# Kernel tuning notes

Measured on AMD Instinct MI355X. Metric: run time of the kernel, lower is better.

## Reference

```python
import jax, jax.numpy as jnp
import numpy as np

B = 4096      # batch (length of the per-sample python loop in the original)
H = 512       # lstm hidden size
A = 18        # nb_action
D = 1024 + A + 1   # lstm / env-embedding dim = 1043
M = 32768     # max_mem_len
K = 32        # ltm_query_breadth
EPS = 1e-5


def _ln(x, g, b):
    m = jnp.mean(x, axis=-1, keepdims=True)
    v = jnp.var(x, axis=-1, keepdims=True)
    return (x - m) / jnp.sqrt(v + EPS) * g + b


def _lstm_cell(x, h, c, W_ih, W_hh, bias):
    # gates: [B, 4H]; split order f, i, o, g (as in the torch module)
    gates = x @ W_ih + h @ W_hh + bias
    f, i, o, g = jnp.split(gates, 4, axis=1)
    c1 = jax.nn.sigmoid(f) * c + jax.nn.sigmoid(i) * jnp.tanh(g)
    h1 = jax.nn.sigmoid(o) * jnp.tanh(c1)
    return h1, c1


def setup_inputs() -> dict:
    key = jax.random.key(0)
    ks = jax.random.split(key, 14)
    f32 = jnp.float32
    return {
        "env_embeddings": jax.random.normal(ks[0], (B, D), f32),
        "hxs": 0.1 * jax.random.normal(ks[1], (B, H), f32),
        "cxs": 0.1 * jax.random.normal(ks[2], (B, H), f32),
        "mem_keys": jax.random.normal(ks[3], (M, H), f32),
        "mem_values": jax.random.normal(ks[4], (M, D), f32),
        "W_ih": 0.02 * jax.random.normal(ks[5], (D, 4 * H), f32),
        "W_hh": 0.02 * jax.random.normal(ks[6], (H, 4 * H), f32),
        "bias": jnp.zeros((4 * H,), f32),
        "ln_g": jnp.ones((H,), f32),
        "ln_b": jnp.zeros((H,), f32),
        "W_critic": 0.02 * jax.random.normal(ks[7], (H, 1), f32),
        "b_critic": jnp.zeros((1,), f32),
        "W_actor": 0.02 * jax.random.normal(ks[8], (H, A), f32),
        "b_actor": jnp.zeros((A,), f32),
        "k": K,
    }


def reference(env_embeddings, hxs, cxs, mem_keys, mem_values,
              W_ih, W_hh, bias, ln_g, ln_b,
              W_critic, b_critic, W_actor, b_actor, k):
    # --- first LSTM pass (batched; per-sample loop in torch is independent) ---
    h1, c1 = _lstm_cell(env_embeddings, hxs, cxs, W_ih, W_hh, bias)

    # --- LTM retrieval: query = layernorm(cell state), top-k attention over memory ---
    q = _ln(c1, ln_g, ln_b)                      # [B, H]
    scores = q @ mem_keys.T                      # [B, M]
    top_vals, inds = jax.lax.top_k(scores, k)    # [B, K]
    weights = jax.nn.softmax(top_vals, axis=-1)  # [B, K]
    gathered = mem_values[inds]                  # [B, K, D]
    memories = jnp.einsum('bk,bkd->bd', weights, gathered)  # [B, D]

    # --- second LSTM pass with retrieved memory as input ---
    h2, c2 = _lstm_cell(memories, h1, c1, W_ih, W_hh, bias)

    critic = h2 @ W_critic + b_critic            # [B, 1]
    actor = h2 @ W_actor + b_actor               # [B, A]
    return critic, actor, h2, c2, inds, weights
```

## Files before the change

kernel.cpp:

```cpp
#include <hip/hip_runtime.h>
#include <hip/hip_bf16.h>
#include <math.h>

#define BATCH 4096
#define HID   512
#define NACT  18
#define DIM   1043
#define MEMN  32768
#define TOPK  32
#define G4H   2048
#define NCHUNK 16
#define CHUNKM (MEMN / NCHUNK)
#define KCP   512

#define OFF_C1   0ull
#define OFF_Q    2097152ull
#define OFF_H1B  4194304ull
#define OFF_PV   5242880ull
#define OFF_PI   7340032ull
#define OFF_MEMB 5242880ull

#define OUT_CRITIC 0
#define OUT_ACTOR  4096
#define OUT_H2     77824
#define OUT_C2     2174976
#define OUT_INDS   4272128
#define OUT_W      4403200

__device__ __forceinline__ float toF_(float x) { return x; }
__device__ __forceinline__ float toF_(__hip_bfloat16 x) { return __bfloat162float(x); }
__device__ __forceinline__ float sigf_(float x) { return 1.0f / (1.0f + expf(-x)); }

__device__ __forceinline__ float np_expf(float x) {
  const float magic = 12582912.0f;
  float q = fmaf(x, 1.442695040888963f, magic) - magic;
  float r = fmaf(q, -6.93145752e-1f, x);
  r = fmaf(q, -1.42860677e-6f, r);
  float num = fmaf(5.082762527590693718096e-04f, r, 6.757896990527504603057e-03f);
  num = fmaf(num, r, 5.114512081637298353406e-02f);
  num = fmaf(num, r, 2.473615434895520810817e-01f);
  num = fmaf(num, r, 7.257664613233124478488e-01f);
  num = fmaf(num, r, 9.999999999980870924916e-01f);
  float den = fmaf(2.159509375685829852307e-02f, r, -2.742335390411667452936e-01f);
  den = fmaf(den, r, 1.0f);
  float poly = __fdiv_rn(num, den);
  int qi = (int)q;
  float scale = __uint_as_float((unsigned)(127 + qi) << 23);
  return __fmul_rn(poly, scale);
}
__device__ __forceinline__ float np_sigmoidf(float x) {
  const float e = np_expf(-x);
  return __fdiv_rn(1.0f, __fadd_rn(1.0f, e));
}
__device__ __forceinline__ float cr_tanhf(float x) { return (float)tanh((double)x); }

template<int PASS, typename TA, typename TC>
__global__ __launch_bounds__(512, 2) void gemm_lstm(
    const TA* __restrict__ A1, const TA* __restrict__ A2,
    const float* __restrict__ W1, const float* __restrict__ W2,
    const float* __restrict__ bias, const TC* __restrict__ cprev,
    float* __restrict__ c1out, __hip_bfloat16* __restrict__ h1b,
    float* __restrict__ outH2, float* __restrict__ outC2)
{
  __shared__ float as[32][66];
  __shared__ float bs[32][132];
  const int tid = threadIdx.x;
  const int b0 = blockIdx.y * 64;
  const int h0 = blockIdx.x * 32;
  const int tr = tid >> 5, tc = tid & 31;
  float accA[4][4] = {};
  float accB[4][4] = {};

  auto run = [&](const TA* __restrict__ A, const float* __restrict__ W,
                 int Ksz, float (&acc)[4][4]) {
    float accP[4][4] = {};
    for (int k0 = 0; k0 < Ksz; k0 += 32) {
      {
        const int r = tid >> 3, kq = tid & 7;
        #pragma unroll
        for (int j = 0; j < 4; ++j) {
          const int kidx = k0 + 4 * kq + j;
          as[4 * kq + j][r] =
              (kidx < Ksz) ? toF_(A[(size_t)(b0 + r) * Ksz + kidx]) : 0.0f;
        }
      }
      {
        const int kk = tid >> 4, sub = tid & 15;
        const bool ok = (k0 + kk) < Ksz;
        #pragma unroll
        for (int g = 0; g < 4; ++g)
          #pragma unroll
          for (int r2 = 0; r2 < 2; ++r2) {
            const float w =
                ok ? W[(size_t)(k0 + kk) * G4H + 512 * g + h0 + 2 * sub + r2] : 0.0f;
            bs[kk][(2 * sub + r2) * 4 + g] = w;
          }
      }
      __syncthreads();
      #pragma unroll
      for (int kk = 0; kk < 32; ++kk) {
        float a[4], b[4];
        #pragma unroll
        for (int u = 0; u < 4; ++u) a[u] = as[kk][4 * tr + u];
        #pragma unroll
        for (int u = 0; u < 4; ++u) b[u] = bs[kk][4 * tc + u];
        #pragma unroll
        for (int jj = 0; jj < 4; ++jj)
          #pragma unroll
          for (int g = 0; g < 4; ++g)
            accP[jj][g] = fmaf(a[jj], b[g], accP[jj][g]);
      }
      __syncthreads();
      if (((k0 + 32) % KCP == 0) || (k0 + 32 >= Ksz)) {
        #pragma unroll
        for (int jj = 0; jj < 4; ++jj)
          #pragma unroll
          for (int g = 0; g < 4; ++g) {
            acc[jj][g] = __fadd_rn(acc[jj][g], accP[jj][g]);
            accP[jj][g] = 0.0f;
          }
      }
    }
  };
  run(A1, W1, DIM, accA);
  run(A2, W2, HID, accB);

  const int h = h0 + tc;
  const float bf = bias[h];
  const float bi = bias[512 + h];
  const float bo = bias[1024 + h];
  const float bg = bias[1536 + h];
  #pragma unroll
  for (int jj = 0; jj < 4; ++jj) {
    const int b = b0 + 4 * tr + jj;
    const float fv = __fadd_rn(__fadd_rn(accA[jj][0], accB[jj][0]), bf);
    const float iv = __fadd_rn(__fadd_rn(accA[jj][1], accB[jj][1]), bi);
    const float ov = __fadd_rn(__fadd_rn(accA[jj][2], accB[jj][2]), bo);
    const float gv = __fadd_rn(__fadd_rn(accA[jj][3], accB[jj][3]), bg);
    const float cp = toF_(cprev[(size_t)b * HID + h]);
    if constexpr (PASS == 1) {
      const float sf = np_sigmoidf(fv);
      const float si = np_sigmoidf(iv);
      const float so = np_sigmoidf(ov);
      const float tg = cr_tanhf(gv);
      const float cn = __fadd_rn(__fmul_rn(sf, cp), __fmul_rn(si, tg));
      const float hn = __fmul_rn(so, cr_tanhf(cn));
      c1out[(size_t)b * HID + h] = cn;
      h1b[(size_t)b * HID + h] = __float2bfloat16(hn);
    } else {
      const float cn = sigf_(fv) * cp + sigf_(iv) * tanhf(gv);
      const float hn = sigf_(ov) * tanhf(cn);
      outC2[(size_t)b * HID + h] = cn;
      outH2[(size_t)b * HID + h] = hn;
    }
  }
}

__global__ __launch_bounds__(256) void ln_q_np(
    const float* __restrict__ c1, const float* __restrict__ ln_g,
    const float* __restrict__ ln_b, float* __restrict__ q)
{
  const int tid = threadIdx.x, lane = tid & 63;
  const int r = blockIdx.x * 4 + (tid >> 6);
  const float* c = c1 + (size_t)r * HID;

  float part;
  {
    const int bi = (lane & 31) >> 3, j = lane & 7;
    const float* p = c + bi * 128 + j;
    float s = p[0];
    #pragma unroll
    for (int k = 1; k < 16; ++k) s = __fadd_rn(s, p[8 * k]);
    part = s;
  }
  part = __fadd_rn(part, __shfl_xor(part, 1, 32));
  part = __fadd_rn(part, __shfl_xor(part, 2, 32));
  part = __fadd_rn(part, __shfl_xor(part, 4, 32));
  part = __fadd_rn(part, __shfl_xor(part, 8, 32));
  part = __fadd_rn(part, __shfl_xor(part, 16, 32));
  const float mean = __fmul_rn(part, 1.0f / 512.0f);

  float part2;
  {
    const int bi = (lane & 31) >> 3, j = lane & 7;
    const float* p = c + bi * 128 + j;
    float d = __fsub_rn(p[0], mean);
    float s = __fmul_rn(d, d);
    #pragma unroll
    for (int k = 1; k < 16; ++k) {
      d = __fsub_rn(p[8 * k], mean);
      s = __fadd_rn(s, __fmul_rn(d, d));
    }
    part2 = s;
  }
  part2 = __fadd_rn(part2, __shfl_xor(part2, 1, 32));
  part2 = __fadd_rn(part2, __shfl_xor(part2, 2, 32));
  part2 = __fadd_rn(part2, __shfl_xor(part2, 4, 32));
  part2 = __fadd_rn(part2, __shfl_xor(part2, 8, 32));
  part2 = __fadd_rn(part2, __shfl_xor(part2, 16, 32));
  const float var = __fmul_rn(part2, 1.0f / 512.0f);

  const float S = __fsqrt_rn(__fadd_rn(var, 1e-5f));
  #pragma unroll
  for (int u = 0; u < 8; ++u) {
    const int i = lane + 64 * u;
    const float dv = __fsub_rn(c[i], mean);
    q[(size_t)r * HID + i] =
        __fadd_rn(__fmul_rn(__fdiv_rn(dv, S), ln_g[i]), ln_b[i]);
  }
}

__global__ __launch_bounds__(512) void score_topk(
    const float* __restrict__ Q, const float* __restrict__ Km,
    float* __restrict__ pv, int* __restrict__ pi)
{
  __shared__ float qs[32][68];
  __shared__ float ks[32][132];
  const int tid = threadIdx.x;
  const int lane = tid & 63;
  const int b0 = blockIdx.y * 64;
  const int chunkBase = blockIdx.x * CHUNKM;
  const int tr = tid >> 5, tc = tid & 31;
  float listV[4];
  int   listI[4];
  #pragma unroll
  for (int j = 0; j < 4; ++j) { listV[j] = -INFINITY; listI[j] = 0; }

  for (int t = 0; t < CHUNKM / 128; ++t) {
    const int m0 = chunkBase + t * 128;
    float acc[4][4] = {};
    for (int k0 = 0; k0 < HID; k0 += 32) {
      {
        const int r = tid >> 3, kq = tid & 7;
        const float4 v = *(const float4*)(Q + (size_t)(b0 + r) * HID + k0 + 4 * kq);
        qs[4 * kq + 0][r] = v.x; qs[4 * kq + 1][r] = v.y;
        qs[4 * kq + 2][r] = v.z; qs[4 * kq + 3][r] = v.w;
      }
      {
        const int col = tid >> 2, sub = tid & 3;
        const float* kp = Km + (size_t)(m0 + col) * HID + k0 + 4 * sub;
        const float4 v0 = *(const float4*)kp;
        const float4 v1 = *(const float4*)(kp + 16);
        ks[4 * sub + 0][col] = v0.x; ks[4 * sub + 1][col] = v0.y;
        ks[4 * sub + 2][col] = v0.z; ks[4 * sub + 3][col] = v0.w;
        ks[16 + 4 * sub + 0][col] = v1.x; ks[16 + 4 * sub + 1][col] = v1.y;
        ks[16 + 4 * sub + 2][col] = v1.z; ks[16 + 4 * sub + 3][col] = v1.w;
      }
      __syncthreads();
      #pragma unroll
      for (int kk = 0; kk < 32; ++kk) {
        const float4 av = *(const float4*)&qs[kk][4 * tr];
        const float4 bv = *(const float4*)&ks[kk][4 * tc];
        const float a[4] = {av.x, av.y, av.z, av.w};
        const float b[4] = {bv.x, bv.y, bv.z, bv.w};
        #pragma unroll
        for (int jj = 0; jj < 4; ++jj)
          #pragma unroll
          for (int cc = 0; cc < 4; ++cc)
            acc[jj][cc] = fmaf(a[jj], b[cc], acc[jj][cc]);
      }
      __syncthreads();
    }
    #pragma unroll
    for (int j = 0; j < 4; ++j) {
      float thr = __shfl(listV[j], (lane < 32) ? 31 : 63);
      float ca[4];
      #pragma unroll
      for (int cc = 0; cc < 4; ++cc) ca[cc] = acc[j][cc];
      while (true) {
        const bool any = (ca[0] > thr) || (ca[1] > thr) ||
                         (ca[2] > thr) || (ca[3] > thr);
        unsigned long long m = __ballot(any);
        if (!m) break;
        const int src = __builtin_ctzll(m);
        const bool participate = ((lane >= 32) == (src >= 32));
        #pragma unroll
        for (int cc = 0; cc < 4; ++cc) {
          const float cv = __shfl(ca[cc], src);
          const float thr_src = __shfl(thr, src);
          if (cv > thr_src) {
            const int ci = m0 + 4 * (src & 31) + cc;
            const unsigned long long em =
                __ballot(participate && (listV[j] < cv));
            if (em) {
              const int pslot = __builtin_ctzll(em) & 31;
              const float shV = __shfl_up(listV[j], 1);
              const int  shI = __shfl_up(listI[j], 1);
              const int slot = lane & 31;
              if (participate && slot >= pslot) {
                listV[j] = (slot == pslot) ? cv : shV;
                listI[j] = (slot == pslot) ? ci : shI;
              }
              thr = __shfl(listV[j], (lane < 32) ? 31 : 63);
            }
          }
        }
        if (lane == src) { ca[0] = ca[1] = ca[2] = ca[3] = -INFINITY; }
      }
    }
  }
  #pragma unroll
  for (int j = 0; j < 4; ++j) {
    const int row = b0 + 8 * (tid >> 6) + j + ((lane >= 32) ? 4 : 0);
    const size_t o = ((size_t)row * NCHUNK + blockIdx.x) * TOPK + (lane & 31);
    pv[o] = listV[j];
    pi[o] = listI[j];
  }
}

__global__ __launch_bounds__(256) void merge_topk(
    const float* __restrict__ pv, const int* __restrict__ pi,
    float* __restrict__ outI, float* __restrict__ outW)
{
  const int tid = threadIdx.x;
  const int lane = tid & 63;
  const int b = blockIdx.x * 4 + (tid >> 6);
  float lv = -INFINITY;
  int li = 0;
  const size_t base = (size_t)b * (NCHUNK * TOPK);
  #pragma unroll
  for (int t = 0; t < (NCHUNK * TOPK) / 64; ++t) {
    const float v = pv[base + t * 64 + lane];
    const int ii = pi[base + t * 64 + lane];
    float thr = __shfl(lv, 31);
    unsigned long long m = __ballot(v > thr);
    while (m) {
      const int src = __builtin_ctzll(m);
      m &= (m - 1);
      const float cv = __shfl(v, src);
      const int ci = __shfl(ii, src);
      if (cv > thr) {
        const unsigned long long em = __ballot((lane < 32) && (lv < cv));
        if (em) {
          const int p = __builtin_ctzll(em);
          const float shV = __shfl_up(lv, 1);
          const int shI = __shfl_up(li, 1);
          if ((lane < 32) && lane >= p) {
            lv = (lane == p) ? cv : shV;
            li = (lane == p) ? ci : shI;
          }
          thr = __shfl(lv, 31);
        }
      }
    }
  }
  const float maxv = __shfl(lv, 0);
  float e = (lane < 32) ? expf(lv - maxv) : 0.0f;
  float s = e;
  #pragma unroll
  for (int d = 1; d < 64; d <<= 1) s += __shfl_xor(s, d);
  const float w = e / s;
  if (lane < 32) {
    outI[(size_t)b * TOPK + lane] = (float)li;
    outW[(size_t)b * TOPK + lane] = w;
  }
}

__global__ __launch_bounds__(256) void gather_mem(
    const float* __restrict__ wf, const float* __restrict__ inf_,
    const float* __restrict__ mv, __hip_bfloat16* __restrict__ memB)
{
  __shared__ float wl[TOPK];
  __shared__ int il[TOPK];
  const int b = blockIdx.x, tid = threadIdx.x;
  if (tid < TOPK) {
    wl[tid] = wf[(size_t)b * TOPK + tid];
    il[tid] = (int)inf_[(size_t)b * TOPK + tid];
  }
  __syncthreads();
  for (int c = tid; c < DIM; c += 256) {
    float acc = 0.0f;
    #pragma unroll
    for (int s = 0; s < TOPK; ++s)
      acc = fmaf(wl[s], mv[(size_t)il[s] * DIM + c], acc);
    memB[(size_t)b * DIM + c] = __float2bfloat16(acc);
  }
}

__global__ __launch_bounds__(256) void heads(
    const float* __restrict__ h2f,
    const float* __restrict__ Wc, const float* __restrict__ bc,
    const float* __restrict__ Wa, const float* __restrict__ ba,
    float* __restrict__ outC, float* __restrict__ outA)
{
  __shared__ float W[HID * 19];
  const int tid = threadIdx.x, lane = tid & 63, wid = tid >> 6;
  for (int idx = tid; idx < HID * 19; idx += 256) {
    const int l = idx / 19, o = idx % 19;
    W[idx] = (o < NACT) ? Wa[l * NACT + o] : Wc[l];
  }
  __syncthreads();
  const int r0 = blockIdx.x * 16 + wid * 4;
  for (int rr = 0; rr < 4; ++rr) {
    const int r = r0 + rr;
    float hv[8];
    #pragma unroll
    for (int u = 0; u < 8; ++u) hv[u] = h2f[(size_t)r * HID + lane + 64 * u];
    for (int o = 0; o < 19; ++o) {
      float s = 0.f;
      #pragma unroll
      for (int u = 0; u < 8; ++u) s = fmaf(hv[u], W[(lane + 64 * u) * 19 + o], s);
      #pragma unroll
      for (int d = 1; d < 64; d <<= 1) s += __shfl_xor(s, d);
      if (lane == 0) {
        if (o < NACT) outA[(size_t)r * NACT + o] = s + ba[o];
        else          outC[r] = s + bc[0];
      }
    }
  }
}

extern "C" void kernel_launch(void* const* d_in, const int* in_sizes, int n_in,
                              void* d_out, int out_size, void* d_ws, size_t ws_size,
                              hipStream_t stream) {
  (void)in_sizes; (void)n_in; (void)out_size; (void)ws_size;
  const float* env    = (const float*)d_in[0];
  const float* hxs    = (const float*)d_in[1];
  const float* cxs    = (const float*)d_in[2];
  const float* mkeys  = (const float*)d_in[3];
  const float* mvals  = (const float*)d_in[4];
  const float* W_ih   = (const float*)d_in[5];
  const float* W_hh   = (const float*)d_in[6];
  const float* bias   = (const float*)d_in[7];
  const float* ln_g   = (const float*)d_in[8];
  const float* ln_b   = (const float*)d_in[9];
  const float* Wc     = (const float*)d_in[10];
  const float* bc     = (const float*)d_in[11];
  const float* Wa     = (const float*)d_in[12];
  const float* ba     = (const float*)d_in[13];

  float* ws = (float*)d_ws;
  float* c1   = ws + OFF_C1;
  float* q    = ws + OFF_Q;
  __hip_bfloat16* h1b = (__hip_bfloat16*)(ws + OFF_H1B);
  float* pv   = ws + OFF_PV;
  int*   pi   = (int*)(ws + OFF_PI);
  __hip_bfloat16* memB = (__hip_bfloat16*)(ws + OFF_MEMB);
  float* out = (float*)d_out;

  gemm_lstm<1, float, float><<<dim3(HID / 32, BATCH / 64), 512, 0, stream>>>(
      env, hxs, W_ih, W_hh, bias, cxs, c1, h1b, nullptr, nullptr);
  ln_q_np<<<BATCH / 4, 256, 0, stream>>>(c1, ln_g, ln_b, q);
  score_topk<<<dim3(NCHUNK, BATCH / 64), 512, 0, stream>>>(q, mkeys, pv, pi);
  merge_topk<<<BATCH / 4, 256, 0, stream>>>(pv, pi, out + OUT_INDS, out + OUT_W);
  gather_mem<<<BATCH, 256, 0, stream>>>(out + OUT_W, out + OUT_INDS, mvals, memB);
  gemm_lstm<2, __hip_bfloat16, float>
      <<<dim3(HID / 32, BATCH / 64), 512, 0, stream>>>(
      memB, h1b, W_ih, W_hh, bias, c1, nullptr, nullptr,
      out + OUT_H2, out + OUT_C2);
  heads<<<BATCH / 16, 256, 0, stream>>>(out + OUT_H2, Wc, bc, Wa, ba,
                                        out + OUT_CRITIC, out + OUT_ACTOR);
}
```

Baseline: 3.995 ms.

## Enlarge score_topk tile to 128x256 with 8x8 register blocking per thread

The fused score+top-k kernel now processes 128 query rows by 256 memory keys per block, with each thread computing an 8x8 accumulator tile instead of 4x4. Shared-memory tiles are padded to avoid bank conflicts, and the per-row streaming top-k insertion logic is adapted to eight rows per half-wave. The aim is to raise FMA-to-LDS-load intensity and halve the global traffic for keys per query row. In exchange, register pressure rises to 64 accumulators plus 16 list registers, the grid halves to 512 blocks, and launch_bounds(512,4) may force spills.

```diff
diff --git a/kernel.cpp b/kernel.cpp
--- a/kernel.cpp
+++ b/kernel.cpp
@@ -210,78 +210,92 @@
   }
 }
 
-__global__ __launch_bounds__(512) void score_topk(
+__global__ __launch_bounds__(512, 4) void score_topk(
     const float* __restrict__ Q, const float* __restrict__ Km,
     float* __restrict__ pv, int* __restrict__ pi)
 {
-  __shared__ float qs[32][68];
-  __shared__ float ks[32][132];
+  __shared__ float as[32][132];
+  __shared__ float bs[32][288];
   const int tid = threadIdx.x;
   const int lane = tid & 63;
-  const int b0 = blockIdx.y * 64;
+  const int w = tid >> 6;
+  const int cg = lane & 31;
+  const int hi = lane >> 5;
+  const int b0 = blockIdx.y * 128;
   const int chunkBase = blockIdx.x * CHUNKM;
-  const int tr = tid >> 5, tc = tid & 31;
-  float listV[4];
-  int   listI[4];
-  #pragma unroll
-  for (int j = 0; j < 4; ++j) { listV[j] = -INFINITY; listI[j] = 0; }
-
-  for (int t = 0; t < CHUNKM / 128; ++t) {
-    const int m0 = chunkBase + t * 128;
-    float acc[4][4] = {};
+  const int rowbase = 16 * w + 8 * hi;
+  const int boff = 8 * cg + 4 * (cg >> 2);
+
+  const int ar = tid & 127;
+  const int akq = tid >> 7;
+  const int bcol = tid >> 1;
+  const int bkq = tid & 1;
+  const int bwo = bcol + 4 * (bcol >> 5);
+
+  float listV[8];
+  int   listI[8];
+  #pragma unroll
+  for (int j = 0; j < 8; ++j) { listV[j] = -INFINITY; listI[j] = 0; }
+
+  for (int t = 0; t < CHUNKM / 256; ++t) {
+    const int m0 = chunkBase + t * 256;
+    float acc[8][8] = {};
     for (int k0 = 0; k0 < HID; k0 += 32) {
       {
-        const int r = tid >> 3, kq = tid & 7;
-        const float4 v = *(const float4*)(Q + (size_t)(b0 + r) * HID + k0 + 4 * kq);
-        qs[4 * kq + 0][r] = v.x; qs[4 * kq + 1][r] = v.y;
-        qs[4 * kq + 2][r] = v.z; qs[4 * kq + 3][r] = v.w;
+        const float* qp = Q + (size_t)(b0 + ar) * HID + k0 + 8 * akq;
+        const float4 v0 = *(const float4*)qp;
+        const float4 v1 = *(const float4*)(qp + 4);
+        as[8 * akq + 0][ar] = v0.x; as[8 * akq + 1][ar] = v0.y;
+        as[8 * akq + 2][ar] = v0.z; as[8 * akq + 3][ar] = v0.w;
+        as[8 * akq + 4][ar] = v1.x; as[8 * akq + 5][ar] = v1.y;
+        as[8 * akq + 6][ar] = v1.z; as[8 * akq + 7][ar] = v1.w;
       }
       {
-        const int col = tid >> 2, sub = tid & 3;
-        const float* kp = Km + (size_t)(m0 + col) * HID + k0 + 4 * sub;
-        const float4 v0 = *(const float4*)kp;
-        const float4 v1 = *(const float4*)(kp + 16);
-        ks[4 * sub + 0][col] = v0.x; ks[4 * sub + 1][col] = v0.y;
-        ks[4 * sub + 2][col] = v0.z; ks[4 * sub + 3][col] = v0.w;
-        ks[16 + 4 * sub + 0][col] = v1.x; ks[16 + 4 * sub + 1][col] = v1.y;
-        ks[16 + 4 * sub + 2][col] = v1.z; ks[16 + 4 * sub + 3][col] = v1.w;
+        const float* kp = Km + (size_t)(m0 + bcol) * HID + k0 + 16 * bkq;
+        #pragma unroll
+        for (int u = 0; u < 4; ++u) {
+          const float4 v = *(const float4*)(kp + 4 * u);
+          bs[16 * bkq + 4 * u + 0][bwo] = v.x;
+          bs[16 * bkq + 4 * u + 1][bwo] = v.y;
+          bs[16 * bkq + 4 * u + 2][bwo] = v.z;
+          bs[16 * bkq + 4 * u + 3][bwo] = v.w;
+        }
       }
       __syncthreads();
       #pragma unroll
       for (int kk = 0; kk < 32; ++kk) {
-        const float4 av = *(const float4*)&qs[kk][4 * tr];
-        const float4 bv = *(const float4*)&ks[kk][4 * tc];
-        const float a[4] = {av.x, av.y, av.z, av.w};
-        const float b[4] = {bv.x, bv.y, bv.z, bv.w};
-        #pragma unroll
-        for (int jj = 0; jj < 4; ++jj)
+        const float4 a0 = *(const float4*)&as[kk][rowbase];
+        const float4 a1 = *(const float4*)&as[kk][rowbase + 4];
+        const float4 bv0 = *(const float4*)&bs[kk][boff];
+        const float4 bv1 = *(const float4*)&bs[kk][boff + 4];
+        const float a[8] = {a0.x, a0.y, a0.z, a0.w, a1.x, a1.y, a1.z, a1.w};
+        const float b[8] = {bv0.x, bv0.y, bv0.z, bv0.w, bv1.x, bv1.y, bv1.z, bv1.w};
+        #pragma unroll
+        for (int j = 0; j < 8; ++j)
           #pragma unroll
-          for (int cc = 0; cc < 4; ++cc)
-            acc[jj][cc] = fmaf(a[jj], b[cc], acc[jj][cc]);
+          for (int c = 0; c < 8; ++c)
+            acc[j][c] = fmaf(a[j], b[c], acc[j][c]);
       }
       __syncthreads();
     }
     #pragma unroll
-    for (int j = 0; j < 4; ++j) {
-      float thr = __shfl(listV[j], (lane < 32) ? 31 : 63);
-      float ca[4];
-      #pragma unroll
-      for (int cc = 0; cc < 4; ++cc) ca[cc] = acc[j][cc];
+    for (int j = 0; j < 8; ++j) {
+      float thr = __shfl(listV[j], hi ? 63 : 31);
       while (true) {
-        const bool any = (ca[0] > thr) || (ca[1] > thr) ||
-                         (ca[2] > thr) || (ca[3] > thr);
+        bool any = false;
+        #pragma unroll
+        for (int c = 0; c < 8; ++c) any = any || (acc[j][c] > thr);
         unsigned long long m = __ballot(any);
         if (!m) break;
         const int src = __builtin_ctzll(m);
-        const bool participate = ((lane >= 32) == (src >= 32));
-        #pragma unroll
-        for (int cc = 0; cc < 4; ++cc) {
-          const float cv = __shfl(ca[cc], src);
+        const bool participate = (hi == (src >> 5));
+        #pragma unroll
+        for (int c = 0; c < 8; ++c) {
+          const float cv = __shfl(acc[j][c], src);
           const float thr_src = __shfl(thr, src);
           if (cv > thr_src) {
-            const int ci = m0 + 4 * (src & 31) + cc;
-            const unsigned long long em =
-                __ballot(participate && (listV[j] < cv));
+            const int ci = m0 + 8 * (src & 31) + c;
+            const unsigned long long em = __ballot(participate && (listV[j] < cv));
             if (em) {
               const int pslot = __builtin_ctzll(em) & 31;
               const float shV = __shfl_up(listV[j], 1);
@@ -291,18 +305,21 @@
                 listV[j] = (slot == pslot) ? cv : shV;
                 listI[j] = (slot == pslot) ? ci : shI;
               }
-              thr = __shfl(listV[j], (lane < 32) ? 31 : 63);
+              thr = __shfl(listV[j], hi ? 63 : 31);
             }
           }
         }
-        if (lane == src) { ca[0] = ca[1] = ca[2] = ca[3] = -INFINITY; }
-      }
-    }
-  }
-  #pragma unroll
-  for (int j = 0; j < 4; ++j) {
-    const int row = b0 + 8 * (tid >> 6) + j + ((lane >= 32) ? 4 : 0);
-    const size_t o = ((size_t)row * NCHUNK + blockIdx.x) * TOPK + (lane & 31);
+        if (lane == src) {
+          #pragma unroll
+          for (int c = 0; c < 8; ++c) acc[j][c] = -INFINITY;
+        }
+      }
+    }
+  }
+  #pragma unroll
+  for (int j = 0; j < 8; ++j) {
+    const int row = b0 + rowbase + j;
+    const size_t o = ((size_t)row * NCHUNK + blockIdx.x) * TOPK + cg;
     pv[o] = listV[j];
     pi[o] = listI[j];
   }
@@ -441,7 +458,7 @@
   gemm_lstm<1, float, float><<<dim3(HID / 32, BATCH / 64), 512, 0, stream>>>(
       env, hxs, W_ih, W_hh, bias, cxs, c1, h1b, nullptr, nullptr);
   ln_q_np<<<BATCH / 4, 256, 0, stream>>>(c1, ln_g, ln_b, q);
-  score_topk<<<dim3(NCHUNK, BATCH / 64), 512, 0, stream>>>(q, mkeys, pv, pi);
+  score_topk<<<dim3(NCHUNK, BATCH / 128), 512, 0, stream>>>(q, mkeys, pv, pi);
   merge_topk<<<BATCH / 4, 256, 0, stream>>>(pv, pi, out + OUT_INDS, out + OUT_W);
   gather_mem<<<BATCH, 256, 0, stream>>>(out + OUT_W, out + OUT_INDS, mvals, memB);
   gemm_lstm<2, __hip_bfloat16, float>
```

New measurement: 4.500 ms. 12.6% more time.
